# Kernel tuning notes

Measured on AMD Instinct MI355X. Metric: run time of the kernel, lower is better.

## Reference

```python
import jax, jax.numpy as jnp
import numpy as np

B, S, D = 4, 2048, 1024
P = 2
N_FEAT = 16          # n_feature_know
N_REST = 16          # n_restore_know
R = 128              # knowledge_rank
D_SPACE = 64


def setup_inputs() -> dict:
    key = jax.random.key(0)
    ks = jax.random.split(key, 6)
    x = jax.random.normal(ks[0], (B, S, D), dtype=jnp.float32)
    # per-token routing weights for each of P feature paths, in [0,1)
    feature_paths = jax.random.uniform(ks[1], (P, B, S, N_FEAT), dtype=jnp.float32)
    f_know = jax.random.normal(ks[2], (N_FEAT, D, R), dtype=jnp.float32) * 0.02
    r_know = jax.random.normal(ks[3], (N_REST, R, D), dtype=jnp.float32) * 0.02
    feature_emb = jax.random.normal(ks[4], (N_FEAT, D_SPACE), dtype=jnp.float32)
    W_router = jax.random.normal(ks[5], (D_SPACE + R, N_REST), dtype=jnp.float32) * 0.05
    return {"x": x, "feature_paths": feature_paths, "f_know": f_know,
            "r_know": r_know, "feature_emb": feature_emb, "W_router": W_router}


def reference(x, feature_paths, f_know, r_know, feature_emb, W_router):
    # Feature projection into all N low-rank banks: [B,S,N,R]
    all_h = jnp.einsum('bsd,ndr->bsnr', x, f_know)
    # Weighted sum over banks per path: [P,B,S,R]
    h_all = jnp.einsum('bsnr,pbsn->pbsr', all_h, feature_paths)
    # Context for restore routing: [P,B,S,D_SPACE]
    neuron_ctx = jnp.einsum('pbsn,nd->pbsd', feature_paths, feature_emb)
    # restore_input = cat([neuron_ctx, h]) -> router -> softmax restore weights
    restore_input = jnp.concatenate([neuron_ctx, h_all], axis=-1)  # [P,B,S,D_SPACE+R]
    logits = jnp.einsum('pbsc,cn->pbsn', restore_input, W_router)
    w = jax.nn.softmax(logits, axis=-1)                            # [P,B,S,N_REST]
    # Restore + per-token weighted combine, summed over P paths: [B,S,D]
    output = jnp.einsum('pbsr,nrd,pbsn->bsd', h_all, r_know, w)
    restore_aux_loss = jnp.float32(0.0)
    return output, restore_aux_loss
```

## Files before the change

kernel.cpp:

```cpp
#include <hip/hip_runtime.h>

typedef __attribute__((ext_vector_type(4))) float f32x4;
typedef __bf16 bf16x8 __attribute__((ext_vector_type(8)));
typedef unsigned short ushort_t;

#define T_TOK 8192
#define DIM   1024
#define NRCOL 2048

#define LGKM0() asm volatile("s_waitcnt lgkmcnt(0)" ::: "memory")
#define VMW(n)  asm volatile("s_waitcnt vmcnt(" #n ")" ::: "memory")
#define SB0()   __builtin_amdgcn_sched_barrier(0)
#define BAR()   __builtin_amdgcn_s_barrier()

static __device__ __forceinline__ unsigned short f2bf(float f) {
  unsigned int u = __builtin_bit_cast(unsigned int, f);
  u += 0x7fffu + ((u >> 16) & 1u);
  return (unsigned short)(u >> 16);
}
static __device__ __forceinline__ float bfbits2f(unsigned int lo16) {
  return __builtin_bit_cast(float, lo16 << 16);
}
static __device__ __forceinline__ void gload16(const void* g, void* l) {
  __builtin_amdgcn_global_load_lds((const __attribute__((address_space(1))) void*)g,
                                   (__attribute__((address_space(3))) void*)l, 16, 0, 0);
}

__global__ __launch_bounds__(256) void cvt_f32_bf16(const float* __restrict__ in,
                                                    unsigned short* __restrict__ out,
                                                    int n4) {
  int i = blockIdx.x * 256 + threadIdx.x;
  const int stride = gridDim.x * 256;
  const float4* in4 = (const float4*)in;
  uint2* o4 = (uint2*)out;
  for (; i < n4; i += stride) {
    float4 v = in4[i];
    uint2 o;
    o.x = (unsigned)f2bf(v.x) | ((unsigned)f2bf(v.y) << 16);
    o.y = (unsigned)f2bf(v.z) | ((unsigned)f2bf(v.w) << 16);
    o4[i] = o;
  }
}

__global__ __launch_bounds__(256) void tcvt(const float* __restrict__ src,
                                            unsigned short* __restrict__ dst,
                                            int rows, int cols,
                                            long sstride, long dstride) {
  src += (size_t)blockIdx.z * sstride;
  dst += (size_t)blockIdx.z * dstride;
  __shared__ float tile[32][33];
  const int tx = threadIdx.x & 31, ty = threadIdx.x >> 5;
  const int r0 = blockIdx.y * 32, c0 = blockIdx.x * 32;
  #pragma unroll
  for (int i = 0; i < 32; i += 8)
    tile[ty + i][tx] = src[(size_t)(r0 + ty + i) * cols + c0 + tx];
  __syncthreads();
  #pragma unroll
  for (int i = 0; i < 32; i += 8)
    dst[(size_t)(c0 + ty + i) * rows + r0 + tx] = f2bf(tile[tx][ty + i]);
}

template<bool OUT_BF16>
__global__ __launch_bounds__(512) void gemm3(const ushort_t* __restrict__ A,
                                             const ushort_t* __restrict__ Bt,
                                             void* __restrict__ Cp,
                                             int N, int K) {
  __shared__ ushort_t As[3][256 * 64];
  __shared__ ushort_t Bs[3][128 * 64];
  const int tid = threadIdx.x;
  const int nx = gridDim.x;
  const int orig = blockIdx.y * nx + blockIdx.x;
  const int q = (nx * gridDim.y) >> 3;
  const int swz = (orig & 7) * q + (orig >> 3);
  const int bx = swz % nx, by = swz / nx;

  const int lane = tid & 63, wv = tid >> 6;
  const int wm = wv >> 1, wn = wv & 1;
  const int lrow = lane & 15, lk = lane >> 4;

  const ushort_t* Ab = A + (size_t)by * 256 * K;
  const ushort_t* Bb = Bt + (size_t)bx * 128 * K;

  auto stageA = [&](int s, int kt, int r) {
    const int off = r * 8192 + tid * 16;
    const int row = off >> 7;
    const int ch = ((off >> 4) & 7) ^ (row & 7);
    gload16(Ab + (size_t)row * K + kt * 64 + ch * 8, (void*)&As[s][off >> 1]);
  };
  auto stageB = [&](int s, int kt, int r) {
    const int off = r * 8192 + tid * 16;
    const int row = off >> 7;
    const int ch = ((off >> 4) & 7) ^ (row & 7);
    gload16(Bb + (size_t)row * K + kt * 64 + ch * 8, (void*)&Bs[s][off >> 1]);
  };

  f32x4 acc[4][4];
  #pragma unroll
  for (int m = 0; m < 4; ++m)
    #pragma unroll
    for (int n = 0; n < 4; ++n)
      acc[m][n] = (f32x4){0.f, 0.f, 0.f, 0.f};

  const int nt = K >> 6;
  #pragma unroll
  for (int r = 0; r < 4; ++r) stageA(0, 0, r);
  #pragma unroll
  for (int r = 0; r < 2; ++r) stageB(0, 0, r);
  #pragma unroll
  for (int r = 0; r < 4; ++r) stageA(1, 1, r);
  #pragma unroll
  for (int r = 0; r < 2; ++r) stageB(1, 1, r);
  VMW(6); SB0(); BAR(); SB0();

  for (int t = 0; t < nt; ++t) {
    const int s = t % 3;
    const int s2 = (t + 2) % 3;
    const bool pf = (t + 2) < nt;
    bf16x8 av[4][2], bv[4][2];
    #pragma unroll
    for (int m = 0; m < 2; ++m)
      #pragma unroll
      for (int ks = 0; ks < 2; ++ks) {
        const int r = wm * 64 + m * 16 + lrow;
        const int ch = (ks * 4 + lk) ^ (r & 7);
        av[m][ks] = *(const bf16x8*)&As[s][r * 64 + ch * 8];
      }
    #pragma unroll
    for (int n = 0; n < 4; ++n)
      #pragma unroll
      for (int ks = 0; ks < 2; ++ks) {
        const int r = wn * 64 + n * 16 + lrow;
        const int ch = (ks * 4 + lk) ^ (r & 7);
        bv[n][ks] = *(const bf16x8*)&Bs[s][r * 64 + ch * 8];
      }
    if (pf) { stageA(s2, t + 2, 0); stageA(s2, t + 2, 1); stageB(s2, t + 2, 0); }
    SB0(); BAR(); LGKM0(); SB0();
    __builtin_amdgcn_s_setprio(1);
    #pragma unroll
    for (int ks = 0; ks < 2; ++ks)
      #pragma unroll
      for (int m = 0; m < 2; ++m)
        #pragma unroll
        for (int n = 0; n < 4; ++n)
          acc[m][n] = __builtin_amdgcn_mfma_f32_16x16x32_bf16(av[m][ks], bv[n][ks], acc[m][n], 0, 0, 0);
    __builtin_amdgcn_s_setprio(0);
    SB0(); BAR(); SB0();
    #pragma unroll
    for (int m = 2; m < 4; ++m)
      #pragma unroll
      for (int ks = 0; ks < 2; ++ks) {
        const int r = wm * 64 + m * 16 + lrow;
        const int ch = (ks * 4 + lk) ^ (r & 7);
        av[m][ks] = *(const bf16x8*)&As[s][r * 64 + ch * 8];
      }
    if (pf) { stageA(s2, t + 2, 2); stageA(s2, t + 2, 3); stageB(s2, t + 2, 1); }
    SB0(); BAR(); LGKM0(); SB0();
    __builtin_amdgcn_s_setprio(1);
    #pragma unroll
    for (int ks = 0; ks < 2; ++ks)
      #pragma unroll
      for (int m = 2; m < 4; ++m)
        #pragma unroll
        for (int n = 0; n < 4; ++n)
          acc[m][n] = __builtin_amdgcn_mfma_f32_16x16x32_bf16(av[m][ks], bv[n][ks], acc[m][n], 0, 0, 0);
    __builtin_amdgcn_s_setprio(0);
    SB0();
    if (pf) { VMW(6); }
    else if (t + 1 < nt) { VMW(0); }
    SB0(); BAR(); SB0();
  }

  #pragma unroll
  for (int m = 0; m < 4; ++m) {
    const int row0 = by * 256 + wm * 64 + m * 16 + lk * 4;
    #pragma unroll
    for (int n = 0; n < 4; ++n) {
      const int col = bx * 128 + wn * 64 + n * 16 + lrow;
      #pragma unroll
      for (int j = 0; j < 4; ++j) {
        const size_t idx = (size_t)(row0 + j) * N + col;
        if constexpr (OUT_BF16) ((ushort_t*)Cp)[idx] = f2bf(acc[m][n][j]);
        else                    ((float*)Cp)[idx] = acc[m][n][j];
      }
    }
  }
}

__global__ __launch_bounds__(256) void middle_kernel(const unsigned short* __restrict__ AH,
                                                     const float* __restrict__ fp,
                                                     const float* __restrict__ femb,
                                                     const float* __restrict__ Wr,
                                                     unsigned short* __restrict__ Mout,
                                                     float* __restrict__ auxout) {
  __shared__ float G[16][16];
  __shared__ float hs[4][2][128];
  __shared__ float wsm[4][2][16];
  const int tid = threadIdx.x;
  {
    const int n = tid >> 4, j = tid & 15;
    float s = 0.f;
    #pragma unroll
    for (int ds = 0; ds < 64; ++ds) s += femb[n * 64 + ds] * Wr[ds * 16 + j];
    G[n][j] = s;
  }
  const int wv = tid >> 6, l = tid & 63;
  const int t = blockIdx.x * 4 + wv;

  float p0[16], p1[16];
  #pragma unroll
  for (int n = 0; n < 16; ++n) {
    p0[n] = fp[t * 16 + n];
    p1[n] = fp[T_TOK * 16 + t * 16 + n];
  }

  float h00 = 0.f, h01 = 0.f, h10 = 0.f, h11 = 0.f;
  const unsigned short* ahrow = AH + (size_t)t * NRCOL;
  #pragma unroll
  for (int n = 0; n < 16; ++n) {
    const unsigned int v = *(const unsigned int*)(ahrow + n * 128 + 2 * l);
    const float a0 = bfbits2f(v & 0xffffu);
    const float a1 = bfbits2f(v >> 16);
    h00 += a0 * p0[n]; h01 += a1 * p0[n];
    h10 += a0 * p1[n]; h11 += a1 * p1[n];
  }
  hs[wv][0][2 * l] = h00; hs[wv][0][2 * l + 1] = h01;
  hs[wv][1][2 * l] = h10; hs[wv][1][2 * l + 1] = h11;
  __syncthreads();

  if (l < 32) {
    const int p = l >> 4, j = l & 15;
    float s = 0.f;
    #pragma unroll
    for (int n = 0; n < 16; ++n) s += (p ? p1[n] : p0[n]) * G[n][j];
    for (int r = 0; r < 128; ++r) s += hs[wv][p][r] * Wr[(64 + r) * 16 + j];
    float mx = s;
    #pragma unroll
    for (int d = 1; d < 16; d <<= 1) mx = fmaxf(mx, __shfl_xor(mx, d, 64));
    const float e = __expf(s - mx);
    float sum = e;
    #pragma unroll
    for (int d = 1; d < 16; d <<= 1) sum += __shfl_xor(sum, d, 64);
    wsm[wv][p][j] = e / sum;
  }
  __syncthreads();

  unsigned short* mrow = Mout + (size_t)t * NRCOL;
  #pragma unroll
  for (int n = 0; n < 16; ++n) {
    const float w0 = wsm[wv][0][n], w1 = wsm[wv][1][n];
    const float m0 = w0 * h00 + w1 * h10;
    const float m1 = w0 * h01 + w1 * h11;
    const unsigned int pk = (unsigned)f2bf(m0) | ((unsigned)f2bf(m1) << 16);
    *(unsigned int*)(mrow + n * 128 + 2 * l) = pk;
  }
  if (blockIdx.x == 0 && tid == 0) auxout[0] = 0.f;
}

extern "C" void kernel_launch(void* const* d_in, const int* in_sizes, int n_in,
                              void* d_out, int out_size, void* d_ws, size_t ws_size,
                              hipStream_t stream) {
  const float* x    = (const float*)d_in[0];
  const float* fp   = (const float*)d_in[1];
  const float* fk   = (const float*)d_in[2];
  const float* rk   = (const float*)d_in[3];
  const float* femb = (const float*)d_in[4];
  const float* Wr   = (const float*)d_in[5];
  float* out = (float*)d_out;

  char* ws = (char*)d_ws;
  unsigned short* Xbf = (unsigned short*)ws;
  unsigned short* W1t = (unsigned short*)(ws + 16u * 1024 * 1024);
  unsigned short* Mb  = (unsigned short*)ws;
  unsigned short* W2t = (unsigned short*)(ws + 32u * 1024 * 1024);
  unsigned short* AH  = (unsigned short*)(ws + 36u * 1024 * 1024);

  cvt_f32_bf16<<<2048, 256, 0, stream>>>(x, Xbf, (T_TOK * DIM) / 4);
  tcvt<<<dim3(128 / 32, 1024 / 32, 16), 256, 0, stream>>>(fk, W1t, 1024, 128,
                                                          1024L * 128, 128L * 1024);
  tcvt<<<dim3(1024 / 32, 2048 / 32, 1), 256, 0, stream>>>(rk, W2t, 2048, 1024, 0, 0);
  gemm3<true><<<dim3(NRCOL / 128, T_TOK / 256), 512, 0, stream>>>(Xbf, W1t, AH,
                                                                  NRCOL, DIM);
  middle_kernel<<<T_TOK / 4, 256, 0, stream>>>(AH, fp, femb, Wr, Mb, out + 8388608);
  gemm3<false><<<dim3(DIM / 128, T_TOK / 256), 512, 0, stream>>>(Mb, W2t, out,
                                                                 DIM, NRCOL);
}
```

Baseline: 126.9 us.

## Replace triple-buffered GEMMs with larger-tile double-buffered GEMM kernels

The first GEMM moves from a 256x128 tile with triple buffering to a 256x256 tile with double buffering. Each wave now computes a 128x64 sub-tile in four interleaved quarter phases, and global-to-LDS prefetches are spread across those phases. The second GEMM gets its own 128x256-tile kernel with the same double-buffer scheme. The aim is higher data reuse per loaded byte and fewer blocks, at the cost of more accumulator registers, fewer resident waves, and less load latency hiding with only two stages.

```diff
diff --git a/kernel.cpp b/kernel.cpp
--- a/kernel.cpp
+++ b/kernel.cpp
@@ -61,12 +61,12 @@
 }
 
 template<bool OUT_BF16>
-__global__ __launch_bounds__(512) void gemm3(const ushort_t* __restrict__ A,
-                                             const ushort_t* __restrict__ Bt,
-                                             void* __restrict__ Cp,
-                                             int N, int K) {
-  __shared__ ushort_t As[3][256 * 64];
-  __shared__ ushort_t Bs[3][128 * 64];
+__global__ __launch_bounds__(512, 2) void gemm4(const ushort_t* __restrict__ A,
+                                                const ushort_t* __restrict__ Bt,
+                                                void* __restrict__ Cp,
+                                                int N, int K) {
+  __shared__ ushort_t As[2][256 * 64];
+  __shared__ ushort_t Bs[2][256 * 64];
   const int tid = threadIdx.x;
   const int nx = gridDim.x;
   const int orig = blockIdx.y * nx + blockIdx.x;
@@ -75,113 +75,244 @@
   const int bx = swz % nx, by = swz / nx;
 
   const int lane = tid & 63, wv = tid >> 6;
-  const int wm = wv >> 1, wn = wv & 1;
+  const int wm = wv >> 2, wn = wv & 3;
   const int lrow = lane & 15, lk = lane >> 4;
+  const int sub8 = lane >> 3, ch8 = lane & 7;
 
   const ushort_t* Ab = A + (size_t)by * 256 * K;
-  const ushort_t* Bb = Bt + (size_t)bx * 128 * K;
-
-  auto stageA = [&](int s, int kt, int r) {
-    const int off = r * 8192 + tid * 16;
-    const int row = off >> 7;
-    const int ch = ((off >> 4) & 7) ^ (row & 7);
-    gload16(Ab + (size_t)row * K + kt * 64 + ch * 8, (void*)&As[s][off >> 1]);
-  };
-  auto stageB = [&](int s, int kt, int r) {
-    const int off = r * 8192 + tid * 16;
-    const int row = off >> 7;
-    const int ch = ((off >> 4) & 7) ^ (row & 7);
-    gload16(Bb + (size_t)row * K + kt * 64 + ch * 8, (void*)&Bs[s][off >> 1]);
-  };
-
-  f32x4 acc[4][4];
-  #pragma unroll
-  for (int m = 0; m < 4; ++m)
+  const ushort_t* Bb = Bt + (size_t)bx * 256 * K;
+
+  auto stA = [&](int s, int kt, int R0) {
+    const int row = R0 + wv * 8 + sub8;
+    const int sc = ch8 ^ (row & 7);
+    gload16(Ab + (size_t)row * K + kt * 64 + sc * 8, (void*)&As[s][row * 64 + ch8 * 8]);
+  };
+  auto stB = [&](int s, int kt, int half, int r) {
+    const int c = r * 8 + wv;
+    const int row = (c >> 2) * 64 + half * 32 + (c & 3) * 8 + sub8;
+    const int sc = ch8 ^ (row & 7);
+    gload16(Bb + (size_t)row * K + kt * 64 + sc * 8, (void*)&Bs[s][row * 64 + ch8 * 8]);
+  };
+  auto rdA = [&](int s, int m, int ks) {
+    const int r = wm * 128 + m * 16 + lrow;
+    const int ch = (ks * 4 + lk) ^ (r & 7);
+    return *(const bf16x8*)&As[s][r * 64 + ch * 8];
+  };
+  auto rdB = [&](int s, int n, int ks) {
+    const int r = wn * 64 + n * 16 + lrow;
+    const int ch = (ks * 4 + lk) ^ (r & 7);
+    return *(const bf16x8*)&Bs[s][r * 64 + ch * 8];
+  };
+
+  f32x4 acc[8][4];
+  #pragma unroll
+  for (int m = 0; m < 8; ++m)
     #pragma unroll
     for (int n = 0; n < 4; ++n)
       acc[m][n] = (f32x4){0.f, 0.f, 0.f, 0.f};
 
   const int nt = K >> 6;
-  #pragma unroll
-  for (int r = 0; r < 4; ++r) stageA(0, 0, r);
-  #pragma unroll
-  for (int r = 0; r < 2; ++r) stageB(0, 0, r);
-  #pragma unroll
-  for (int r = 0; r < 4; ++r) stageA(1, 1, r);
-  #pragma unroll
-  for (int r = 0; r < 2; ++r) stageB(1, 1, r);
+  stA(0, 0, 0); stA(0, 0, 128); stA(0, 0, 64); stA(0, 0, 192);
+  stB(0, 0, 0, 0); stB(0, 0, 0, 1); stB(0, 0, 1, 0); stB(0, 0, 1, 1);
+  stA(1, 1, 0); stA(1, 1, 128);
+  stB(1, 1, 0, 0); stB(1, 1, 0, 1); stB(1, 1, 1, 0); stB(1, 1, 1, 1);
   VMW(6); SB0(); BAR(); SB0();
 
   for (int t = 0; t < nt; ++t) {
-    const int s = t % 3;
-    const int s2 = (t + 2) % 3;
-    const bool pf = (t + 2) < nt;
-    bf16x8 av[4][2], bv[4][2];
-    #pragma unroll
-    for (int m = 0; m < 2; ++m)
-      #pragma unroll
-      for (int ks = 0; ks < 2; ++ks) {
-        const int r = wm * 64 + m * 16 + lrow;
-        const int ch = (ks * 4 + lk) ^ (r & 7);
-        av[m][ks] = *(const bf16x8*)&As[s][r * 64 + ch * 8];
-      }
-    #pragma unroll
-    for (int n = 0; n < 4; ++n)
-      #pragma unroll
-      for (int ks = 0; ks < 2; ++ks) {
-        const int r = wn * 64 + n * 16 + lrow;
-        const int ch = (ks * 4 + lk) ^ (r & 7);
-        bv[n][ks] = *(const bf16x8*)&Bs[s][r * 64 + ch * 8];
-      }
-    if (pf) { stageA(s2, t + 2, 0); stageA(s2, t + 2, 1); stageB(s2, t + 2, 0); }
+    const int s = t & 1, so = s ^ 1;
+    bf16x8 av1[4][2], av2[4][2], bv1[2][2], bv2[2][2];
+    #pragma unroll
+    for (int m = 0; m < 4; ++m)
+      #pragma unroll
+      for (int ks = 0; ks < 2; ++ks) av1[m][ks] = rdA(s, m, ks);
+    #pragma unroll
+    for (int n = 0; n < 2; ++n)
+      #pragma unroll
+      for (int ks = 0; ks < 2; ++ks) bv1[n][ks] = rdB(s, n, ks);
+    if (t + 1 < nt) { stA(so, t + 1, 64); stA(so, t + 1, 192); }
     SB0(); BAR(); LGKM0(); SB0();
     __builtin_amdgcn_s_setprio(1);
     #pragma unroll
     for (int ks = 0; ks < 2; ++ks)
       #pragma unroll
-      for (int m = 0; m < 2; ++m)
-        #pragma unroll
-        for (int n = 0; n < 4; ++n)
-          acc[m][n] = __builtin_amdgcn_mfma_f32_16x16x32_bf16(av[m][ks], bv[n][ks], acc[m][n], 0, 0, 0);
-    __builtin_amdgcn_s_setprio(0);
-    SB0(); BAR(); SB0();
-    #pragma unroll
-    for (int m = 2; m < 4; ++m)
-      #pragma unroll
-      for (int ks = 0; ks < 2; ++ks) {
-        const int r = wm * 64 + m * 16 + lrow;
-        const int ch = (ks * 4 + lk) ^ (r & 7);
-        av[m][ks] = *(const bf16x8*)&As[s][r * 64 + ch * 8];
-      }
-    if (pf) { stageA(s2, t + 2, 2); stageA(s2, t + 2, 3); stageB(s2, t + 2, 1); }
+      for (int m = 0; m < 4; ++m)
+        #pragma unroll
+        for (int n = 0; n < 2; ++n)
+          acc[m][n] = __builtin_amdgcn_mfma_f32_16x16x32_bf16(av1[m][ks], bv1[n][ks], acc[m][n], 0, 0, 0);
+    __builtin_amdgcn_s_setprio(0);
+    SB0(); BAR(); SB0();
+    #pragma unroll
+    for (int n = 0; n < 2; ++n)
+      #pragma unroll
+      for (int ks = 0; ks < 2; ++ks) bv2[n][ks] = rdB(s, n + 2, ks);
+    if (t + 2 < nt) { stA(s, t + 2, 0); stA(s, t + 2, 128); }
     SB0(); BAR(); LGKM0(); SB0();
     __builtin_amdgcn_s_setprio(1);
     #pragma unroll
     for (int ks = 0; ks < 2; ++ks)
       #pragma unroll
-      for (int m = 2; m < 4; ++m)
-        #pragma unroll
-        for (int n = 0; n < 4; ++n)
-          acc[m][n] = __builtin_amdgcn_mfma_f32_16x16x32_bf16(av[m][ks], bv[n][ks], acc[m][n], 0, 0, 0);
-    __builtin_amdgcn_s_setprio(0);
+      for (int m = 0; m < 4; ++m)
+        #pragma unroll
+        for (int n = 0; n < 2; ++n)
+          acc[m][n + 2] = __builtin_amdgcn_mfma_f32_16x16x32_bf16(av1[m][ks], bv2[n][ks], acc[m][n + 2], 0, 0, 0);
+    __builtin_amdgcn_s_setprio(0);
+    SB0(); BAR(); SB0();
+    #pragma unroll
+    for (int m = 0; m < 4; ++m)
+      #pragma unroll
+      for (int ks = 0; ks < 2; ++ks) av2[m][ks] = rdA(s, m + 4, ks);
+    if (t + 2 < nt) { stB(s, t + 2, 0, 0); stB(s, t + 2, 0, 1); }
+    SB0(); BAR(); LGKM0(); SB0();
+    __builtin_amdgcn_s_setprio(1);
+    #pragma unroll
+    for (int ks = 0; ks < 2; ++ks)
+      #pragma unroll
+      for (int m = 0; m < 4; ++m)
+        #pragma unroll
+        for (int n = 0; n < 2; ++n)
+          acc[m + 4][n] = __builtin_amdgcn_mfma_f32_16x16x32_bf16(av2[m][ks], bv1[n][ks], acc[m + 4][n], 0, 0, 0);
+    __builtin_amdgcn_s_setprio(0);
+    SB0(); BAR(); SB0();
+    if (t + 2 < nt) { stB(s, t + 2, 1, 0); stB(s, t + 2, 1, 1); }
     SB0();
-    if (pf) { VMW(6); }
-    else if (t + 1 < nt) { VMW(0); }
-    SB0(); BAR(); SB0();
-  }
-
-  #pragma unroll
-  for (int m = 0; m < 4; ++m) {
-    const int row0 = by * 256 + wm * 64 + m * 16 + lk * 4;
+    __builtin_amdgcn_s_setprio(1);
+    #pragma unroll
+    for (int ks = 0; ks < 2; ++ks)
+      #pragma unroll
+      for (int m = 0; m < 4; ++m)
+        #pragma unroll
+        for (int n = 0; n < 2; ++n)
+          acc[m + 4][n + 2] = __builtin_amdgcn_mfma_f32_16x16x32_bf16(av2[m][ks], bv2[n][ks], acc[m + 4][n + 2], 0, 0, 0);
+    __builtin_amdgcn_s_setprio(0);
+    SB0();
+    if (t + 2 < nt) { VMW(6); } else { VMW(0); }
+    SB0(); BAR(); SB0();
+  }
+
+  #pragma unroll
+  for (int m = 0; m < 8; ++m) {
+    const int row0 = by * 256 + wm * 128 + m * 16 + lk * 4;
     #pragma unroll
     for (int n = 0; n < 4; ++n) {
-      const int col = bx * 128 + wn * 64 + n * 16 + lrow;
+      const int col = bx * 256 + wn * 64 + n * 16 + lrow;
       #pragma unroll
       for (int j = 0; j < 4; ++j) {
         const size_t idx = (size_t)(row0 + j) * N + col;
         if constexpr (OUT_BF16) ((ushort_t*)Cp)[idx] = f2bf(acc[m][n][j]);
         else                    ((float*)Cp)[idx] = acc[m][n][j];
       }
+    }
+  }
+}
+
+__global__ __launch_bounds__(512, 2) void gemm2p(const ushort_t* __restrict__ A,
+                                                 const ushort_t* __restrict__ Bt,
+                                                 float* __restrict__ Cp,
+                                                 int N, int K) {
+  __shared__ ushort_t As[2][128 * 64];
+  __shared__ ushort_t Bs[2][256 * 64];
+  const int tid = threadIdx.x;
+  const int nx = gridDim.x;
+  const int orig = blockIdx.y * nx + blockIdx.x;
+  const int q = (nx * gridDim.y) >> 3;
+  const int swz = (orig & 7) * q + (orig >> 3);
+  const int bx = swz % nx, by = swz / nx;
+
+  const int lane = tid & 63, wv = tid >> 6;
+  const int wm = wv >> 2, wn = wv & 3;
+  const int lrow = lane & 15, lk = lane >> 4;
+  const int sub8 = lane >> 3, ch8 = lane & 7;
+
+  const ushort_t* Ab = A + (size_t)by * 128 * K;
+  const ushort_t* Bb = Bt + (size_t)bx * 256 * K;
+
+  auto stA = [&](int s, int kt, int R0) {
+    const int row = R0 + wv * 8 + sub8;
+    const int sc = ch8 ^ (row & 7);
+    gload16(Ab + (size_t)row * K + kt * 64 + sc * 8, (void*)&As[s][row * 64 + ch8 * 8]);
+  };
+  auto stB = [&](int s, int kt, int half, int r) {
+    const int c = r * 8 + wv;
+    const int row = (c >> 2) * 64 + half * 32 + (c & 3) * 8 + sub8;
+    const int sc = ch8 ^ (row & 7);
+    gload16(Bb + (size_t)row * K + kt * 64 + sc * 8, (void*)&Bs[s][row * 64 + ch8 * 8]);
+  };
+  auto rdA = [&](int s, int m, int ks) {
+    const int r = wm * 64 + m * 16 + lrow;
+    const int ch = (ks * 4 + lk) ^ (r & 7);
+    return *(const bf16x8*)&As[s][r * 64 + ch * 8];
+  };
+  auto rdB = [&](int s, int n, int ks) {
+    const int r = wn * 64 + n * 16 + lrow;
+    const int ch = (ks * 4 + lk) ^ (r & 7);
+    return *(const bf16x8*)&Bs[s][r * 64 + ch * 8];
+  };
+
+  f32x4 acc[4][4];
+  #pragma unroll
+  for (int m = 0; m < 4; ++m)
+    #pragma unroll
+    for (int n = 0; n < 4; ++n)
+      acc[m][n] = (f32x4){0.f, 0.f, 0.f, 0.f};
+
+  const int nt = K >> 6;
+  stA(0, 0, 0); stA(0, 0, 64);
+  stB(0, 0, 0, 0); stB(0, 0, 0, 1); stB(0, 0, 1, 0); stB(0, 0, 1, 1);
+  stA(1, 1, 0); stA(1, 1, 64); stB(1, 1, 0, 0);
+  VMW(3); SB0(); BAR(); SB0();
+
+  for (int t = 0; t < nt; ++t) {
+    const int s = t & 1, so = s ^ 1;
+    bf16x8 av[4][2], bv1[2][2], bv2[2][2];
+    #pragma unroll
+    for (int m = 0; m < 4; ++m)
+      #pragma unroll
+      for (int ks = 0; ks < 2; ++ks) av[m][ks] = rdA(s, m, ks);
+    #pragma unroll
+    for (int n = 0; n < 2; ++n)
+      #pragma unroll
+      for (int ks = 0; ks < 2; ++ks) bv1[n][ks] = rdB(s, n, ks);
+    if (t + 1 < nt) { stB(so, t + 1, 1, 0); stB(so, t + 1, 1, 1); stB(so, t + 1, 0, 1); }
+    SB0(); BAR(); LGKM0(); SB0();
+    __builtin_amdgcn_s_setprio(1);
+    #pragma unroll
+    for (int ks = 0; ks < 2; ++ks)
+      #pragma unroll
+      for (int m = 0; m < 4; ++m)
+        #pragma unroll
+        for (int n = 0; n < 2; ++n)
+          acc[m][n] = __builtin_amdgcn_mfma_f32_16x16x32_bf16(av[m][ks], bv1[n][ks], acc[m][n], 0, 0, 0);
+    __builtin_amdgcn_s_setprio(0);
+    SB0(); BAR(); SB0();
+    #pragma unroll
+    for (int n = 0; n < 2; ++n)
+      #pragma unroll
+      for (int ks = 0; ks < 2; ++ks) bv2[n][ks] = rdB(s, n + 2, ks);
+    if (t + 2 < nt) { stA(s, t + 2, 0); stA(s, t + 2, 64); stB(s, t + 2, 0, 0); }
+    SB0(); BAR(); LGKM0(); SB0();
+    __builtin_amdgcn_s_setprio(1);
+    #pragma unroll
+    for (int ks = 0; ks < 2; ++ks)
+      #pragma unroll
+      for (int m = 0; m < 4; ++m)
+        #pragma unroll
+        for (int n = 0; n < 2; ++n)
+          acc[m][n + 2] = __builtin_amdgcn_mfma_f32_16x16x32_bf16(av[m][ks], bv2[n][ks], acc[m][n + 2], 0, 0, 0);
+    __builtin_amdgcn_s_setprio(0);
+    SB0();
+    if (t + 2 < nt) { VMW(3); } else { VMW(0); }
+    SB0(); BAR(); SB0();
+  }
+
+  #pragma unroll
+  for (int m = 0; m < 4; ++m) {
+    const int row0 = by * 128 + wm * 64 + m * 16 + lk * 4;
+    #pragma unroll
+    for (int n = 0; n < 4; ++n) {
+      const int col = bx * 256 + wn * 64 + n * 16 + lrow;
+      #pragma unroll
+      for (int j = 0; j < 4; ++j)
+        Cp[(size_t)(row0 + j) * N + col] = acc[m][n][j];
     }
   }
 }
@@ -278,9 +409,9 @@
   tcvt<<<dim3(128 / 32, 1024 / 32, 16), 256, 0, stream>>>(fk, W1t, 1024, 128,
                                                           1024L * 128, 128L * 1024);
   tcvt<<<dim3(1024 / 32, 2048 / 32, 1), 256, 0, stream>>>(rk, W2t, 2048, 1024, 0, 0);
-  gemm3<true><<<dim3(NRCOL / 128, T_TOK / 256), 512, 0, stream>>>(Xbf, W1t, AH,
+  gemm4<true><<<dim3(NRCOL / 256, T_TOK / 256), 512, 0, stream>>>(Xbf, W1t, AH,
                                                                   NRCOL, DIM);
   middle_kernel<<<T_TOK / 4, 256, 0, stream>>>(AH, fp, femb, Wr, Mb, out + 8388608);
-  gemm3<false><<<dim3(DIM / 128, T_TOK / 256), 512, 0, stream>>>(Mb, W2t, out,
-                                                                 DIM, NRCOL);
-}
+  gemm2p<<<dim3(DIM / 256, T_TOK / 128), 512, 0, stream>>>(Mb, W2t, out,
+                                                           DIM, NRCOL);
+}
```

After: 117.9 us. 7.1% less time.
